# Optimization experiments

Hardware: AMD Instinct MI355X
Metric: run time of the kernel (lower is better)

The kernel has to match this reference:

```python
import jax, jax.numpy as jnp
import numpy as np

N, K, D = 262144, 1024, 64


def setup_inputs() -> dict:
    key = jax.random.key(0)
    k1, k2 = jax.random.split(key)
    input_data = jax.random.normal(k1, (N, D), dtype=jnp.float32)
    codewords = jax.random.normal(k2, (K, D), dtype=jnp.float32)
    return {"input_data": input_data, "codewords": codewords}


def reference(input_data, codewords):
    # input_data: [N, D], codewords: [K, D]
    x = input_data.reshape(-1, codewords.shape[1])
    x2 = jnp.sum(x * x, axis=1, keepdims=True)          # [N, 1]
    c2 = jnp.sum(codewords * codewords, axis=1)          # [K]
    d2 = x2 + c2[None, :] - 2.0 * (x @ codewords.T)      # [N, K]
    distances = jnp.sqrt(jnp.maximum(d2, 0.0))
    quantized_indices = jnp.argmin(distances, axis=1)    # [N] int
    quantized_distances = jnp.take_along_axis(
        distances, quantized_indices[:, None], axis=1
    )[:, 0]                                              # [N]
    quantized_data = codewords[quantized_indices]        # [N, D]
    return (quantized_indices, quantized_distances, quantized_data)
```

## Files before the change

kernel.cpp:

```cpp
#include <hip/hip_runtime.h>


#define N_PTS 262144
#define K_CW  1024
#define DIM   64

typedef __attribute__((ext_vector_type(8)))  short short8;
typedef __attribute__((ext_vector_type(16))) float floatx16;

__device__ __forceinline__ unsigned short f2bf(float f) {
    unsigned u = __float_as_uint(f);
    return (unsigned short)((u + 0x7FFFu + ((u >> 16) & 1u)) >> 16);
}
__device__ __forceinline__ float bf2f(unsigned short h) {
    return __uint_as_float(((unsigned)h) << 16);
}
__device__ __forceinline__ float dot4(float4 a, float4 b) {
    return a.x*b.x + a.y*b.y + a.z*b.z + a.w*b.w;
}

__launch_bounds__(256, 2)
__global__ void vq_kernel(const float* __restrict__ x,
                          const float* __restrict__ cw,
                          float* __restrict__ out) {
    __shared__ __align__(16) unsigned short sB[2 * 128 * 72];
    __shared__ float sc2[128];
    __shared__ int   sci[512];
    __shared__ float sdd[512];
    __shared__ int   sidx[256];

    const int tid  = threadIdx.x;
    const int w    = tid >> 6;
    const int lane = tid & 63;
    const int q    = lane >> 5;
    const int l31  = lane & 31;
    const int base = blockIdx.x * 256;
    const float4* __restrict__ x4  = (const float4*)x;
    const float4* __restrict__ c4p = (const float4*)cw;

    short8 ah[2][4], al[2][4];
    #pragma unroll
    for (int rt = 0; rt < 2; ++rt) {
        const int row = w * 64 + rt * 32 + l31;
        const float4* xr = x4 + (size_t)(base + row) * 16;
        #pragma unroll
        for (int ks = 0; ks < 4; ++ks) {
            float4 va = xr[ks * 4 + q * 2];
            float4 vb = xr[ks * 4 + q * 2 + 1];
            float f[8] = {va.x, va.y, va.z, va.w, vb.x, vb.y, vb.z, vb.w};
            short8 h, l;
            #pragma unroll
            for (int j = 0; j < 8; ++j) {
                unsigned short hb = f2bf(f[j]);
                h[j] = (short)hb;
                l[j] = (short)f2bf(f[j] - bf2f(hb));
            }
            ah[rt][ks] = h; al[rt][ks] = l;
        }
    }

    float bs[32]; int bi[32];
    #pragma unroll
    for (int s = 0; s < 32; ++s) { bs[s] = 3.4e38f; bi[s] = 0; }

    for (int ch = 0; ch < 8; ++ch) {
        __syncthreads();
        {
            const float4* cg = c4p + ch * 2048;
            #pragma unroll
            for (int i = 0; i < 8; ++i) {
                const int g = i * 256 + tid;
                const int row = g >> 4, c4 = g & 15;
                float4 v = cg[g];
                unsigned short h0 = f2bf(v.x), h1 = f2bf(v.y), h2 = f2bf(v.z), h3 = f2bf(v.w);
                unsigned short l0 = f2bf(v.x - bf2f(h0)), l1 = f2bf(v.y - bf2f(h1)),
                               l2 = f2bf(v.z - bf2f(h2)), l3 = f2bf(v.w - bf2f(h3));
                uint2 hv, lv;
                hv.x = (unsigned)h0 | ((unsigned)h1 << 16);
                hv.y = (unsigned)h2 | ((unsigned)h3 << 16);
                lv.x = (unsigned)l0 | ((unsigned)l1 << 16);
                lv.y = (unsigned)l2 | ((unsigned)l3 << 16);
                *(uint2*)&sB[row * 72 + c4 * 4]        = hv;
                *(uint2*)&sB[9216 + row * 72 + c4 * 4] = lv;
                float part = dot4(v, v);
                part += __shfl_xor(part, 1);
                part += __shfl_xor(part, 2);
                part += __shfl_xor(part, 4);
                part += __shfl_xor(part, 8);
                if (c4 == 0) sc2[row] = part;
            }
        }
        __syncthreads();

        #pragma unroll
        for (int ct = 0; ct < 4; ++ct) {
            const int nrow = ct * 32 + l31;
            short8 bh[4], bl[4];
            #pragma unroll
            for (int ks = 0; ks < 4; ++ks) {
                bh[ks] = *(const short8*)&sB[nrow * 72 + ks * 16 + q * 8];
                bl[ks] = *(const short8*)&sB[9216 + nrow * 72 + ks * 16 + q * 8];
            }
            floatx16 a0, a1;
            #pragma unroll
            for (int r = 0; r < 16; ++r) { a0[r] = 0.f; a1[r] = 0.f; }
            #pragma unroll
            for (int ks = 0; ks < 4; ++ks) {
                a0 = __builtin_amdgcn_mfma_f32_32x32x16_bf16(ah[0][ks], bh[ks], a0, 0, 0, 0);
                a1 = __builtin_amdgcn_mfma_f32_32x32x16_bf16(ah[1][ks], bh[ks], a1, 0, 0, 0);
                a0 = __builtin_amdgcn_mfma_f32_32x32x16_bf16(al[0][ks], bh[ks], a0, 0, 0, 0);
                a1 = __builtin_amdgcn_mfma_f32_32x32x16_bf16(al[1][ks], bh[ks], a1, 0, 0, 0);
                a0 = __builtin_amdgcn_mfma_f32_32x32x16_bf16(ah[0][ks], bl[ks], a0, 0, 0, 0);
                a1 = __builtin_amdgcn_mfma_f32_32x32x16_bf16(ah[1][ks], bl[ks], a1, 0, 0, 0);
            }
            const float c2v  = sc2[nrow];
            const int   idxv = ch * 128 + nrow;
            #pragma unroll
            for (int r = 0; r < 16; ++r) {
                float s0 = fmaf(-2.f, a0[r], c2v);
                bool lt0 = s0 < bs[r];
                bs[r] = lt0 ? s0 : bs[r];
                bi[r] = lt0 ? idxv : bi[r];
                float s1 = fmaf(-2.f, a1[r], c2v);
                bool lt1 = s1 < bs[16 + r];
                bs[16 + r] = lt1 ? s1 : bs[16 + r];
                bi[16 + r] = lt1 ? idxv : bi[16 + r];
            }
        }
    }

    #pragma unroll
    for (int s = 0; s < 32; ++s) {
        float b0 = bs[s]; int i0 = bi[s];
        float b1 = 3.4e38f; int i1 = 0x7fffffff;
        #pragma unroll
        for (int m = 1; m < 32; m <<= 1) {
            float ob0 = __shfl_xor(b0, m); int oi0 = __shfl_xor(i0, m);
            float ob1 = __shfl_xor(b1, m); int oi1 = __shfl_xor(i1, m);
            bool t = (ob0 < b0) || (ob0 == b0 && oi0 < i0);
            float hs = t ? b0 : ob0; int hi_ = t ? i0 : oi0;
            b0 = t ? ob0 : b0;       i0 = t ? oi0 : i0;
            bool u = (ob1 < b1) || (ob1 == b1 && oi1 < i1);
            float ms = u ? ob1 : b1; int mi = u ? oi1 : i1;
            bool z = (hs < ms) || (hs == ms && hi_ < mi);
            b1 = z ? hs : ms; i1 = z ? hi_ : mi;
        }
        if (l31 == s) {
            const int rt = s >> 4, r = s & 15;
            const int row = w * 64 + rt * 32 + (r & 3) + 8 * (r >> 2) + 4 * q;
            sci[row * 2]     = i0;
            sci[row * 2 + 1] = i1;
        }
    }
    __syncthreads();

    #pragma unroll
    for (int it = 0; it < 2; ++it) {
        const int pid = it * 128 + (tid >> 1);
        const int h   = tid & 1;
        const int ia = sci[pid * 2], ib = sci[pid * 2 + 1];
        const float4* xr = x4 + (size_t)(base + pid) * 16 + h * 8;
        const float4* ca = c4p + (size_t)ia * 16 + h * 8;
        const float4* cb = c4p + (size_t)ib * 16 + h * 8;
        float da = 0.f, db = 0.f;
        #pragma unroll
        for (int j = 0; j < 8; ++j) {
            float4 xv = xr[j], av = ca[j], bv = cb[j];
            float4 d1 = make_float4(xv.x-av.x, xv.y-av.y, xv.z-av.z, xv.w-av.w);
            float4 d2 = make_float4(xv.x-bv.x, xv.y-bv.y, xv.z-bv.z, xv.w-bv.w);
            da += dot4(d1, d1);
            db += dot4(d2, d2);
        }
        da += __shfl_xor(da, 1);
        db += __shfl_xor(db, 1);
        if (h == 0) { sdd[pid * 2] = da; sdd[pid * 2 + 1] = db; }
    }
    __syncthreads();

    {
        const float da = sdd[tid * 2], db = sdd[tid * 2 + 1];
        const int   ia = sci[tid * 2], ib = sci[tid * 2 + 1];
        bool ta = (da < db) || (da == db && ia < ib);
        const int   bidx = ta ? ia : ib;
        const float bd   = ta ? da : db;
        out[base + tid]         = (float)bidx;
        out[N_PTS + base + tid] = sqrtf(fmaxf(bd, 0.f));
        sidx[tid] = bidx;
    }
    __syncthreads();

    {
        float4* od = (float4*)(out + 2 * (size_t)N_PTS) + (size_t)base * 16;
        #pragma unroll
        for (int i = 0; i < 16; ++i) {
            const int g = i * 256 + tid;
            od[g] = c4p[(size_t)sidx[g >> 4] * 16 + (g & 15)];
        }
    }
}

extern "C" void kernel_launch(void* const* d_in, const int* in_sizes, int n_in,
                              void* d_out, int out_size, void* d_ws, size_t ws_size,
                              hipStream_t stream) {
    const float* x  = (const float*)d_in[0];
    const float* cw = (const float*)d_in[1];
    float* out = (float*)d_out;
    vq_kernel<<<N_PTS / 256, 256, 0, stream>>>(x, cw, out);
}
```

Baseline: 281.2 us.

## Precompute bf16 codeword split in prep kernel and double-buffer async LDS loads

Adds a small prep kernel that converts the codewords once into a hi/lo bf16 padded layout and precomputes their squared norms in the workspace. The main kernel then streams each 128-codeword chunk straight into LDS with global_load_lds into a double buffer, prefetching the next chunk while the MFMAs run on the current one. This removes the per-block repeated fp32→bf16 conversion, the shuffle reductions and one barrier per chunk. In exchange it adds an extra launch, doubles the LDS footprint, and relies on the async-copy completion being ordered correctly by the barrier.

```diff
diff --git a/kernel.cpp b/kernel.cpp
--- a/kernel.cpp
+++ b/kernel.cpp
@@ -4,6 +4,8 @@
 #define N_PTS 262144
 #define K_CW  1024
 #define DIM   64
+#define CHUNK_B 36864
+#define C2_OFF  (8 * CHUNK_B)
 
 typedef __attribute__((ext_vector_type(8)))  short short8;
 typedef __attribute__((ext_vector_type(16))) float floatx16;
@@ -18,16 +20,47 @@
 __device__ __forceinline__ float dot4(float4 a, float4 b) {
     return a.x*b.x + a.y*b.y + a.z*b.z + a.w*b.w;
 }
+__device__ __forceinline__ void async_cp16(const void* g, void* l) {
+    __builtin_amdgcn_global_load_lds(
+        (const __attribute__((address_space(1))) unsigned int*)g,
+        (__attribute__((address_space(3))) unsigned int*)l, 16, 0, 0);
+}
+
+__global__ void vq_prep(const float* __restrict__ cw, unsigned char* __restrict__ ws) {
+    const int k = blockIdx.x * 256 + threadIdx.x;
+    const int ch = k >> 7, r = k & 127;
+    unsigned short* chunk = (unsigned short*)(ws + (size_t)ch * CHUNK_B);
+    unsigned short* hi = chunk + r * 72;
+    unsigned short* lo = hi + 9216;
+    const float4* cr = (const float4*)cw + (size_t)k * 16;
+    float c2 = 0.f;
+    #pragma unroll
+    for (int j = 0; j < 16; ++j) {
+        float4 v = cr[j];
+        c2 += dot4(v, v);
+        unsigned short h0 = f2bf(v.x), h1 = f2bf(v.y), h2 = f2bf(v.z), h3 = f2bf(v.w);
+        unsigned short l0 = f2bf(v.x - bf2f(h0)), l1 = f2bf(v.y - bf2f(h1)),
+                       l2 = f2bf(v.z - bf2f(h2)), l3 = f2bf(v.w - bf2f(h3));
+        uint2 hv, lv;
+        hv.x = (unsigned)h0 | ((unsigned)h1 << 16);
+        hv.y = (unsigned)h2 | ((unsigned)h3 << 16);
+        lv.x = (unsigned)l0 | ((unsigned)l1 << 16);
+        lv.y = (unsigned)l2 | ((unsigned)l3 << 16);
+        *(uint2*)(hi + j * 4) = hv;
+        *(uint2*)(lo + j * 4) = lv;
+    }
+    ((float*)(ws + C2_OFF))[k] = c2;
+}
 
 __launch_bounds__(256, 2)
 __global__ void vq_kernel(const float* __restrict__ x,
                           const float* __restrict__ cw,
+                          const unsigned char* __restrict__ ws,
                           float* __restrict__ out) {
-    __shared__ __align__(16) unsigned short sB[2 * 128 * 72];
-    __shared__ float sc2[128];
-    __shared__ int   sci[512];
-    __shared__ float sdd[512];
-    __shared__ int   sidx[256];
+    __shared__ __align__(16) unsigned char sB[2 * CHUNK_B];
+    int*   sci  = (int*)sB;
+    float* sdd  = (float*)(sB + 2048);
+    int*   sidx = (int*)(sB + 4096);
 
     const int tid  = threadIdx.x;
     const int w    = tid >> 6;
@@ -37,6 +70,7 @@
     const int base = blockIdx.x * 256;
     const float4* __restrict__ x4  = (const float4*)x;
     const float4* __restrict__ c4p = (const float4*)cw;
+    const float*  __restrict__ c2g = (const float*)(ws + C2_OFF);
 
     short8 ah[2][4], al[2][4];
     #pragma unroll
@@ -63,34 +97,28 @@
     #pragma unroll
     for (int s = 0; s < 32; ++s) { bs[s] = 3.4e38f; bi[s] = 0; }
 
+    {
+        const unsigned char* g = ws + w * 9216 + lane * 16;
+        unsigned char* l = sB + w * 9216;
+        #pragma unroll
+        for (int i = 0; i < 9; ++i) async_cp16(g + i * 1024, l + i * 1024);
+    }
+
     for (int ch = 0; ch < 8; ++ch) {
         __syncthreads();
-        {
-            const float4* cg = c4p + ch * 2048;
-            #pragma unroll
-            for (int i = 0; i < 8; ++i) {
-                const int g = i * 256 + tid;
-                const int row = g >> 4, c4 = g & 15;
-                float4 v = cg[g];
-                unsigned short h0 = f2bf(v.x), h1 = f2bf(v.y), h2 = f2bf(v.z), h3 = f2bf(v.w);
-                unsigned short l0 = f2bf(v.x - bf2f(h0)), l1 = f2bf(v.y - bf2f(h1)),
-                               l2 = f2bf(v.z - bf2f(h2)), l3 = f2bf(v.w - bf2f(h3));
-                uint2 hv, lv;
-                hv.x = (unsigned)h0 | ((unsigned)h1 << 16);
-                hv.y = (unsigned)h2 | ((unsigned)h3 << 16);
-                lv.x = (unsigned)l0 | ((unsigned)l1 << 16);
-                lv.y = (unsigned)l2 | ((unsigned)l3 << 16);
-                *(uint2*)&sB[row * 72 + c4 * 4]        = hv;
-                *(uint2*)&sB[9216 + row * 72 + c4 * 4] = lv;
-                float part = dot4(v, v);
-                part += __shfl_xor(part, 1);
-                part += __shfl_xor(part, 2);
-                part += __shfl_xor(part, 4);
-                part += __shfl_xor(part, 8);
-                if (c4 == 0) sc2[row] = part;
-            }
-        }
-        __syncthreads();
+
+        if (ch < 7) {
+            const unsigned char* g = ws + (size_t)(ch + 1) * CHUNK_B + w * 9216 + lane * 16;
+            unsigned char* l = sB + ((ch + 1) & 1) * CHUNK_B + w * 9216;
+            #pragma unroll
+            for (int i = 0; i < 9; ++i) async_cp16(g + i * 1024, l + i * 1024);
+        }
+
+        float c2v[4];
+        #pragma unroll
+        for (int ct = 0; ct < 4; ++ct) c2v[ct] = c2g[ch * 128 + ct * 32 + l31];
+
+        const unsigned short* bufS = (const unsigned short*)(sB + (ch & 1) * CHUNK_B);
 
         #pragma unroll
         for (int ct = 0; ct < 4; ++ct) {
@@ -98,8 +126,8 @@
             short8 bh[4], bl[4];
             #pragma unroll
             for (int ks = 0; ks < 4; ++ks) {
-                bh[ks] = *(const short8*)&sB[nrow * 72 + ks * 16 + q * 8];
-                bl[ks] = *(const short8*)&sB[9216 + nrow * 72 + ks * 16 + q * 8];
+                bh[ks] = *(const short8*)&bufS[nrow * 72 + ks * 16 + q * 8];
+                bl[ks] = *(const short8*)&bufS[9216 + nrow * 72 + ks * 16 + q * 8];
             }
             floatx16 a0, a1;
             #pragma unroll
@@ -113,21 +141,21 @@
                 a0 = __builtin_amdgcn_mfma_f32_32x32x16_bf16(ah[0][ks], bl[ks], a0, 0, 0, 0);
                 a1 = __builtin_amdgcn_mfma_f32_32x32x16_bf16(ah[1][ks], bl[ks], a1, 0, 0, 0);
             }
-            const float c2v  = sc2[nrow];
-            const int   idxv = ch * 128 + nrow;
+            const int idxv = ch * 128 + nrow;
             #pragma unroll
             for (int r = 0; r < 16; ++r) {
-                float s0 = fmaf(-2.f, a0[r], c2v);
+                float s0 = fmaf(-2.f, a0[r], c2v[ct]);
                 bool lt0 = s0 < bs[r];
                 bs[r] = lt0 ? s0 : bs[r];
                 bi[r] = lt0 ? idxv : bi[r];
-                float s1 = fmaf(-2.f, a1[r], c2v);
+                float s1 = fmaf(-2.f, a1[r], c2v[ct]);
                 bool lt1 = s1 < bs[16 + r];
                 bs[16 + r] = lt1 ? s1 : bs[16 + r];
                 bi[16 + r] = lt1 ? idxv : bi[16 + r];
             }
         }
     }
+    __syncthreads();
 
     #pragma unroll
     for (int s = 0; s < 32; ++s) {
@@ -205,5 +233,7 @@
     const float* x  = (const float*)d_in[0];
     const float* cw = (const float*)d_in[1];
     float* out = (float*)d_out;
-    vq_kernel<<<N_PTS / 256, 256, 0, stream>>>(x, cw, out);
-}
+    unsigned char* ws = (unsigned char*)d_ws;
+    vq_prep<<<4, 256, 0, stream>>>(cw, ws);
+    vq_kernel<<<N_PTS / 256, 256, 0, stream>>>(x, cw, ws, out);
+}
```

Result: faster. 254.6 us (-9.4%).
